# Optimization experiments

Hardware: AMD Instinct MI355X
Metric: run time of the kernel (lower is better)

Reference implementation:

```python
import jax, jax.numpy as jnp
import numpy as np

DOWNSAMPLE = 512  # points per cloud, from init_kwargs


def _pairwise_dist(x, y):
    """Batched Euclidean distance matrix. x: (B,n,D), y: (B,m,D) -> (B,n,m)."""
    x2 = jnp.sum(x * x, axis=-1)                     # (B,n)
    y2 = jnp.sum(y * y, axis=-1)                     # (B,m)
    d2 = x2[:, :, None] + y2[:, None, :] - 2.0 * jnp.einsum('bnd,bmd->bnm', x, y)
    pos = d2 > 0.0                                   # guard sqrt(0)/negatives from fp error
    return jnp.where(pos, jnp.sqrt(jnp.where(pos, d2, 1.0)), 0.0)


def setup_inputs() -> dict:
    key = jax.random.key(0)
    k1, k2 = jax.random.split(key)
    inp = jax.random.normal(k1, (65536, 128), dtype=jnp.float32)
    tgt = jax.random.normal(k2, (65536, 128), dtype=jnp.float32)
    return {"input": inp, "target": tgt}


def reference(input, target):
    D = input.shape[-1]
    x = input.reshape(-1, DOWNSAMPLE, D)   # (B, n, D)
    y = target.reshape(-1, DOWNSAMPLE, D)  # (B, n, D)
    # geomloss energy kernel loss with uniform weights:
    # L_b = mean||x-y|| - 0.5*mean||x-x'|| - 0.5*mean||y-y'||
    cross = jnp.mean(_pairwise_dist(x, y), axis=(1, 2))  # (B,)
    xx = jnp.mean(_pairwise_dist(x, x), axis=(1, 2))
    yy = jnp.mean(_pairwise_dist(y, y), axis=(1, 2))
    loss = cross - 0.5 * xx - 0.5 * yy
    return jnp.mean(loss)
```

## Files before the change

### kernel.cpp

```cpp
#include <hip/hip_runtime.h>

typedef __attribute__((ext_vector_type(8))) __bf16 bf16x8;
typedef __attribute__((ext_vector_type(4))) float f32x4;
typedef __attribute__((ext_vector_type(8))) unsigned short ushort8;
typedef __attribute__((ext_vector_type(4))) unsigned short u16x4;

#define DSAMP 512
#define DIM   128
#define S1    ((size_t)16777216)
#define REG5  16384
#define NBPB  36
#define WS_NEEDED ((size_t)(4 * S1 + 2 * 262144 + 128 * NBPB * 4))

__global__ __launch_bounds__(256)
void presplit3(const float* __restrict__ x, const float* __restrict__ y,
               char* __restrict__ ws) {
    __shared__ __align__(16) char img[4 * 8192];
    __shared__ float nrm[64];

    const int tid = threadIdx.x;
    const int nb  = gridDim.x >> 1;
    const int input = (blockIdx.x >= nb) ? 1 : 0;
    const int rb    = blockIdx.x - input * nb;

    const float* src = (input ? y : x) + (size_t)rb * 64 * DIM;

    #pragma unroll
    for (int i = 0; i < 8; ++i) {
        int f  = i * 256 + tid;
        int r  = f >> 5;
        int k4 = f & 31;
        float4 v = ((const float4*)src)[f];

        float s = v.x * v.x + v.y * v.y + v.z * v.z + v.w * v.w;
        #pragma unroll
        for (int o = 16; o > 0; o >>= 1) s += __shfl_down(s, o, 32);
        if ((tid & 31) == 0) nrm[r] = s;

        float xs[4] = {v.x, v.y, v.z, v.w};
        u16x4 hv, lv;
        #pragma unroll
        for (int e = 0; e < 4; ++e) {
            float xv = xs[e];
            unsigned ub = __float_as_uint(xv);
            unsigned hr = (ub + 0x7fffu + ((ub >> 16) & 1u)) >> 16;
            float hf = __uint_as_float(hr << 16);
            float rs = xv - hf;
            unsigned ul = __float_as_uint(rs);
            unsigned lr = (ul + 0x7fffu + ((ul >> 16) & 1u)) >> 16;
            hv[e] = (unsigned short)hr;
            lv[e] = (unsigned short)lr;
        }
        int c  = k4 >> 4;
        int q  = k4 & 15;
        int jb = q >> 1;
        int h  = q & 1;
        int addr = r * 128 + ((jb ^ (r & 7)) * 16) + h * 8;
        *(u16x4*)(img + (size_t)(0 + c) * 8192 + addr) = hv;
        *(u16x4*)(img + (size_t)(2 + c) * 8192 + addr) = lv;
    }
    __syncthreads();

    const int wv = tid >> 6, lane = tid & 63;
    const int hl = wv >> 1, ch = wv & 1;
    const int b     = rb >> 3;
    const int rowin = (rb & 7) * 64;
    char* gdst = ws + (size_t)input * 2 * S1 + (size_t)hl * S1
               + ((size_t)(b * 2 + ch) * 512 + rowin) * 128;
    const char* lsrc = img + (size_t)wv * 8192;
    #pragma unroll
    for (int j = 0; j < 8; ++j) {
        int o = (j * 64 + lane) * 16;
        *(float4*)(gdst + o) = *(const float4*)(lsrc + o);
    }
    if (tid < 64) {
        float* nG = (float*)(ws + 4 * S1) + (size_t)input * 65536 + rb * 64;
        nG[tid] = nrm[tid];
    }
}

__global__ __launch_bounds__(256, 3)
void mmd_tile5(const char* __restrict__ ws, float* __restrict__ partials) {
    __shared__ __align__(16) char smem[3 * REG5];
    __shared__ float Pn[128];
    __shared__ float Qn[128];
    __shared__ float wred[4];

    const int tid = threadIdx.x;
    const int xcd = blockIdx.x & 7;
    const int seq = blockIdx.x >> 3;
    const int b   = xcd + 8 * (seq / NBPB);
    const int s   = seq % NBPB;

    int type, ti, tj; float w; bool diag;
    if (s < 16) { type = 0; ti = s >> 2; tj = s & 3; w = 1.0f; diag = false; }
    else {
        int u = s - 16;
        type = 1 + (u >= 10);
        if (u >= 10) u -= 10;
        int i = (u >= 4) + (u >= 7) + (u >= 9);
        int off = (i == 1) ? 4 : (i == 2) ? 7 : (i == 3) ? 9 : 0;
        int j = u - off + i;
        ti = i; tj = j; diag = (i == j); w = diag ? -0.5f : -1.0f;
    }

    const char* Xhi = ws;
    const char* Yhi = ws + 2 * S1;
    const float* normX = (const float*)(ws + 4 * S1);
    const float* normY = normX + 65536;

    const char* Phi = (type == 2) ? Yhi : Xhi;
    const char* Qhi = (type == 1) ? Xhi : Yhi;
    const float* nP = (type == 2) ? normY : normX;
    const float* nQ = (type == 1) ? normX : normY;

    if (tid < 128) Pn[tid]       = nP[(size_t)b * 512 + ti * 128 + tid];
    else           Qn[tid - 128] = nQ[(size_t)b * 512 + tj * 128 + (tid - 128)];

    const int lane    = tid & 63;
    const int wv      = tid >> 6;
    const int rowHalf = (wv >> 1) * 64;
    const int colHalf = (wv & 1) * 64;
    const int fm      = lane & 15;
    const int kq      = lane >> 4;
    const int sw      = fm & 7;

    f32x4 acc[4][4];
    #pragma unroll
    for (int a2 = 0; a2 < 4; ++a2)
        #pragma unroll
        for (int b2 = 0; b2 < 4; ++b2)
            acc[a2][b2] = (f32x4){0.f, 0.f, 0.f, 0.f};

    for (int c = 0; c < 2; ++c) {
        if (c) __syncthreads();
        {
            size_t chrow = (size_t)(b * 2 + c) * 512;
            const char* srcs[3];
            srcs[0] = Phi + (chrow + (size_t)ti * 128) * 128;
            srcs[1] = Qhi + (chrow + (size_t)tj * 128) * 128;
            srcs[2] = srcs[1] + S1;
            #pragma unroll
            for (int f = 0; f < 12; ++f) {
                int g = wv * 12 + f;
                int region = g >> 4;
                int sub    = g & 15;
                const char* gs = srcs[region] + sub * 1024 + lane * 16;
                char* ls = smem + (size_t)region * REG5 + sub * 1024 + lane * 16;
                __builtin_amdgcn_global_load_lds(
                    (const __attribute__((address_space(1))) void*)gs,
                    (__attribute__((address_space(3))) void*)ls, 16, 0, 0);
            }
        }
        __syncthreads();
        #pragma unroll
        for (int ks = 0; ks < 2; ++ks) {
            const int jx = ((ks * 4 + kq) ^ sw) * 16;
            bf16x8 ah[4], bh[4], bl[4];
            #pragma unroll
            for (int a2 = 0; a2 < 4; ++a2) {
                int ar = rowHalf + a2 * 16 + fm;
                ah[a2] = *(const bf16x8*)(smem + ar * 128 + jx);
            }
            #pragma unroll
            for (int b2 = 0; b2 < 4; ++b2) {
                int br = colHalf + b2 * 16 + fm;
                bh[b2] = *(const bf16x8*)(smem + REG5     + br * 128 + jx);
                bl[b2] = *(const bf16x8*)(smem + 2 * REG5 + br * 128 + jx);
            }
            #pragma unroll
            for (int a2 = 0; a2 < 4; ++a2)
                #pragma unroll
                for (int b2 = 0; b2 < 4; ++b2) {
                    acc[a2][b2] = __builtin_amdgcn_mfma_f32_16x16x32_bf16(ah[a2], bh[b2], acc[a2][b2], 0, 0, 0);
                    acc[a2][b2] = __builtin_amdgcn_mfma_f32_16x16x32_bf16(ah[a2], bl[b2], acc[a2][b2], 0, 0, 0);
                }
        }
    }

    float Pr[16], Qc[4];
    #pragma unroll
    for (int a2 = 0; a2 < 4; ++a2)
        #pragma unroll
        for (int rg = 0; rg < 4; ++rg)
            Pr[a2 * 4 + rg] = Pn[rowHalf + a2 * 16 + kq * 4 + rg];
    #pragma unroll
    for (int b2 = 0; b2 < 4; ++b2) Qc[b2] = Qn[colHalf + b2 * 16 + fm];

    float lsum = 0.f;
    #pragma unroll
    for (int a2 = 0; a2 < 4; ++a2) {
        #pragma unroll
        for (int b2 = 0; b2 < 4; ++b2) {
            #pragma unroll
            for (int rg = 0; rg < 4; ++rg) {
                float d2 = fmaf(-2.0f, acc[a2][b2][rg], Pr[a2 * 4 + rg] + Qc[b2]);
                float v  = __builtin_amdgcn_sqrtf(fmaxf(d2, 0.0f));
                if (diag && (rowHalf + a2 * 16 + kq * 4 + rg) == (colHalf + b2 * 16 + fm))
                    v = 0.f;
                lsum += v;
            }
        }
    }
    #pragma unroll
    for (int off = 32; off > 0; off >>= 1) lsum += __shfl_down(lsum, off, 64);
    if (lane == 0) wred[wv] = lsum;
    __syncthreads();
    if (tid == 0)
        partials[blockIdx.x] = (wred[0] + wred[1] + wred[2] + wred[3]) * w;
}

__global__ __launch_bounds__(256, 2)
void mmd_tile_fallback(const float* __restrict__ x, const float* __restrict__ y,
                       float* __restrict__ partials) {
    __shared__ __align__(16) char smem[4 * 128 * 144];
    __shared__ float Pn[128];
    __shared__ float Qn[128];
    __shared__ float wred[4];

    char* Ah = smem;
    char* Al = smem + 1 * 128 * 144;
    char* Bh = smem + 2 * 128 * 144;
    char* Bl = smem + 3 * 128 * 144;

    const int tid  = threadIdx.x;
    const int bid  = blockIdx.x;
    const int tj   = bid & 3;
    const int ti   = (bid >> 2) & 3;
    const int type = (bid >> 4) % 3;
    const int b    = bid / 48;

    const float* Xb = x + (size_t)b * DSAMP * DIM;
    const float* Yb = y + (size_t)b * DSAMP * DIM;
    const float* Pp; const float* Qp; float w;
    if (type == 0)      { Pp = Xb; Qp = Yb; w = 1.0f;  }
    else if (type == 1) { Pp = Xb; Qp = Xb; w = -0.5f; }
    else                { Pp = Yb; Qp = Yb; w = -0.5f; }
    Pp += (size_t)ti * 128 * DIM;
    Qp += (size_t)tj * 128 * DIM;

    {
        const float* rp = (tid < 128) ? (Pp + (size_t)tid * DIM)
                                      : (Qp + (size_t)(tid - 128) * DIM);
        float s = 0.f;
        #pragma unroll
        for (int k4 = 0; k4 < 32; ++k4) {
            float4 v = ((const float4*)rp)[k4];
            s += v.x * v.x + v.y * v.y + v.z * v.z + v.w * v.w;
        }
        if (tid < 128) Pn[tid] = s; else Qn[tid - 128] = s;
    }

    const int lane    = tid & 63;
    const int wv      = tid >> 6;
    const int rowHalf = (wv >> 1) * 64;
    const int colHalf = (wv & 1) * 64;
    const int fm      = lane & 15;
    const int kq      = lane >> 4;

    f32x4 acc[4][4];
    #pragma unroll
    for (int a2 = 0; a2 < 4; ++a2)
        #pragma unroll
        for (int b2 = 0; b2 < 4; ++b2)
            acc[a2][b2] = (f32x4){0.f, 0.f, 0.f, 0.f};

    for (int c = 0; c < 2; ++c) {
        if (c) __syncthreads();
        #pragma unroll
        for (int side = 0; side < 2; ++side) {
            const float* sp = side ? Qp : Pp;
            char* dh = side ? Bh : Ah;
            char* dl = side ? Bl : Al;
            #pragma unroll
            for (int it = 0; it < 4; ++it) {
                int u  = it * 256 + tid;
                int r  = u >> 3;
                int c8 = u & 7;
                const float* g = sp + (size_t)r * DIM + c * 64 + c8 * 8;
                float4 v0 = ((const float4*)g)[0];
                float4 v1 = ((const float4*)g)[1];
                float xs[8] = {v0.x, v0.y, v0.z, v0.w, v1.x, v1.y, v1.z, v1.w};
                ushort8 hv, lv;
                #pragma unroll
                for (int e = 0; e < 8; ++e) {
                    float xv = xs[e];
                    unsigned ub = __float_as_uint(xv);
                    unsigned hr = (ub + 0x7fffu + ((ub >> 16) & 1u)) >> 16;
                    float hf = __uint_as_float(hr << 16);
                    float rs = xv - hf;
                    unsigned ul = __float_as_uint(rs);
                    unsigned lr = (ul + 0x7fffu + ((ul >> 16) & 1u)) >> 16;
                    hv[e] = (unsigned short)hr;
                    lv[e] = (unsigned short)lr;
                }
                *(ushort8*)(dh + r * 144 + c8 * 16) = hv;
                *(ushort8*)(dl + r * 144 + c8 * 16) = lv;
            }
        }
        __syncthreads();
        #pragma unroll
        for (int ks = 0; ks < 2; ++ks) {
            const int kb2 = (ks * 32 + kq * 8) * 2;
            bf16x8 ah[4], al[4], bh[4], bl[4];
            #pragma unroll
            for (int a2 = 0; a2 < 4; ++a2) {
                int ar = rowHalf + a2 * 16 + fm;
                ah[a2] = *(const bf16x8*)(Ah + ar * 144 + kb2);
                al[a2] = *(const bf16x8*)(Al + ar * 144 + kb2);
            }
            #pragma unroll
            for (int b2 = 0; b2 < 4; ++b2) {
                int br = colHalf + b2 * 16 + fm;
                bh[b2] = *(const bf16x8*)(Bh + br * 144 + kb2);
                bl[b2] = *(const bf16x8*)(Bl + br * 144 + kb2);
            }
            #pragma unroll
            for (int a2 = 0; a2 < 4; ++a2)
                #pragma unroll
                for (int b2 = 0; b2 < 4; ++b2) {
                    acc[a2][b2] = __builtin_amdgcn_mfma_f32_16x16x32_bf16(ah[a2], bh[b2], acc[a2][b2], 0, 0, 0);
                    acc[a2][b2] = __builtin_amdgcn_mfma_f32_16x16x32_bf16(ah[a2], bl[b2], acc[a2][b2], 0, 0, 0);
                    acc[a2][b2] = __builtin_amdgcn_mfma_f32_16x16x32_bf16(al[a2], bh[b2], acc[a2][b2], 0, 0, 0);
                }
        }
    }

    const bool selfm = (type != 0) && (ti == tj);
    float lsum = 0.f;
    #pragma unroll
    for (int a2 = 0; a2 < 4; ++a2) {
        int ib = rowHalf + a2 * 16 + kq * 4;
        #pragma unroll
        for (int b2 = 0; b2 < 4; ++b2) {
            int j = colHalf + b2 * 16 + fm;
            float qn = Qn[j];
            #pragma unroll
            for (int rg = 0; rg < 4; ++rg) {
                int i = ib + rg;
                float d2 = Pn[i] + qn - 2.0f * acc[a2][b2][rg];
                if (d2 > 0.f && !(selfm && i == j)) lsum += sqrtf(d2);
            }
        }
    }
    #pragma unroll
    for (int off = 32; off > 0; off >>= 1) lsum += __shfl_down(lsum, off, 64);
    if (lane == 0) wred[wv] = lsum;
    __syncthreads();
    if (tid == 0)
        partials[bid] = (wred[0] + wred[1] + wred[2] + wred[3]) * w;
}

__global__ __launch_bounds__(256)
void mmd_finalize_kernel(const float* __restrict__ partials, int n,
                         float* __restrict__ out, double scale) {
    __shared__ double sh[256];
    double s = 0.0;
    for (int i = threadIdx.x; i < n; i += 256) s += (double)partials[i];
    sh[threadIdx.x] = s;
    __syncthreads();
    for (int off = 128; off > 0; off >>= 1) {
        if ((int)threadIdx.x < off) sh[threadIdx.x] += sh[threadIdx.x + off];
        __syncthreads();
    }
    if (threadIdx.x == 0) out[0] = (float)(sh[0] * scale);
}

extern "C" void kernel_launch(void* const* d_in, const int* in_sizes, int n_in,
                              void* d_out, int out_size, void* d_ws, size_t ws_size,
                              hipStream_t stream) {
    const float* x = (const float*)d_in[0];
    const float* y = (const float*)d_in[1];
    float* out = (float*)d_out;

    const int n = in_sizes[0];
    const int B = n / (DSAMP * DIM);
    const double scale = 1.0 / ((double)B * (double)DSAMP * (double)DSAMP);

    if (ws_size >= WS_NEEDED) {
        char* ws = (char*)d_ws;
        float* partials = (float*)(ws + 4 * S1 + 2 * 262144);
        const int nb = (n / DIM) / 64;
        const int nblocks = B * NBPB;
        presplit3<<<dim3(2 * nb), dim3(256), 0, stream>>>(x, y, ws);
        mmd_tile5<<<dim3(nblocks), dim3(256), 0, stream>>>(ws, partials);
        mmd_finalize_kernel<<<dim3(1), dim3(256), 0, stream>>>(partials, nblocks, out, scale);
    } else {
        float* partials = (float*)d_ws;
        const int nblocks = B * 48;
        mmd_tile_fallback<<<dim3(nblocks), dim3(256), 0, stream>>>(x, y, partials);
        mmd_finalize_kernel<<<dim3(1), dim3(256), 0, stream>>>(partials, nblocks, out, scale);
    }
}
```

Measured before the change: 153.3 us.

## Load low-half B operand directly from global and simplify presplit kernel

The tile kernel no longer stages the low-order bf16 part of the Q operand in LDS. Each wave reads it straight from global memory into registers before the barrier, which cuts LDS to two regions and raises the occupancy hint from 3 to 4 blocks per CU. The presplit kernel drops its LDS staging and instead has each thread write swizzled hi/lo halves and norms directly to global memory. The trade-off is uncoalesced 8-byte global writes in presplit, and per-wave redundant, less-coalesced global reads of the lo tile in place of shared LDS reuse.

```diff
diff --git a/kernel.cpp b/kernel.cpp
--- a/kernel.cpp
+++ b/kernel.cpp
@@ -13,75 +13,59 @@
 #define WS_NEEDED ((size_t)(4 * S1 + 2 * 262144 + 128 * NBPB * 4))
 
 __global__ __launch_bounds__(256)
-void presplit3(const float* __restrict__ x, const float* __restrict__ y,
+void presplit4(const float* __restrict__ x, const float* __restrict__ y,
                char* __restrict__ ws) {
-    __shared__ __align__(16) char img[4 * 8192];
-    __shared__ float nrm[64];
-
     const int tid = threadIdx.x;
-    const int nb  = gridDim.x >> 1;
-    const int input = (blockIdx.x >= nb) ? 1 : 0;
-    const int rb    = blockIdx.x - input * nb;
-
-    const float* src = (input ? y : x) + (size_t)rb * 64 * DIM;
-
-    #pragma unroll
-    for (int i = 0; i < 8; ++i) {
-        int f  = i * 256 + tid;
-        int r  = f >> 5;
-        int k4 = f & 31;
-        float4 v = ((const float4*)src)[f];
-
-        float s = v.x * v.x + v.y * v.y + v.z * v.z + v.w * v.w;
-        #pragma unroll
-        for (int o = 16; o > 0; o >>= 1) s += __shfl_down(s, o, 32);
-        if ((tid & 31) == 0) nrm[r] = s;
-
-        float xs[4] = {v.x, v.y, v.z, v.w};
-        u16x4 hv, lv;
-        #pragma unroll
-        for (int e = 0; e < 4; ++e) {
-            float xv = xs[e];
-            unsigned ub = __float_as_uint(xv);
-            unsigned hr = (ub + 0x7fffu + ((ub >> 16) & 1u)) >> 16;
-            float hf = __uint_as_float(hr << 16);
-            float rs = xv - hf;
-            unsigned ul = __float_as_uint(rs);
-            unsigned lr = (ul + 0x7fffu + ((ul >> 16) & 1u)) >> 16;
-            hv[e] = (unsigned short)hr;
-            lv[e] = (unsigned short)lr;
-        }
-        int c  = k4 >> 4;
-        int q  = k4 & 15;
-        int jb = q >> 1;
-        int h  = q & 1;
-        int addr = r * 128 + ((jb ^ (r & 7)) * 16) + h * 8;
-        *(u16x4*)(img + (size_t)(0 + c) * 8192 + addr) = hv;
-        *(u16x4*)(img + (size_t)(2 + c) * 8192 + addr) = lv;
-    }
-    __syncthreads();
-
-    const int wv = tid >> 6, lane = tid & 63;
-    const int hl = wv >> 1, ch = wv & 1;
-    const int b     = rb >> 3;
-    const int rowin = (rb & 7) * 64;
-    char* gdst = ws + (size_t)input * 2 * S1 + (size_t)hl * S1
-               + ((size_t)(b * 2 + ch) * 512 + rowin) * 128;
-    const char* lsrc = img + (size_t)wv * 8192;
-    #pragma unroll
-    for (int j = 0; j < 8; ++j) {
-        int o = (j * 64 + lane) * 16;
-        *(float4*)(gdst + o) = *(const float4*)(lsrc + o);
-    }
-    if (tid < 64) {
-        float* nG = (float*)(ws + 4 * S1) + (size_t)input * 65536 + rb * 64;
-        nG[tid] = nrm[tid];
-    }
-}
-
-__global__ __launch_bounds__(256, 3)
-void mmd_tile5(const char* __restrict__ ws, float* __restrict__ partials) {
-    __shared__ __align__(16) char smem[3 * REG5];
+    const size_t fidx = (size_t)blockIdx.x * 256 + tid;
+    const int r   = (int)(fidx >> 5);
+    const int k4  = (int)(fidx & 31);
+    const int input = r >> 16;
+    const int ri    = r & 65535;
+
+    const float* src = input ? y : x;
+    float4 v = ((const float4*)src)[((size_t)ri << 5) + k4];
+
+    float s = v.x * v.x + v.y * v.y + v.z * v.z + v.w * v.w;
+    #pragma unroll
+    for (int o = 16; o > 0; o >>= 1) s += __shfl_down(s, o, 32);
+
+    float xs[4] = {v.x, v.y, v.z, v.w};
+    u16x4 hv, lv;
+    #pragma unroll
+    for (int e = 0; e < 4; ++e) {
+        float xv = xs[e];
+        unsigned ub = __float_as_uint(xv);
+        unsigned hr = (ub + 0x7fffu + ((ub >> 16) & 1u)) >> 16;
+        float hf = __uint_as_float(hr << 16);
+        float rs = xv - hf;
+        unsigned ul = __float_as_uint(rs);
+        unsigned lr = (ul + 0x7fffu + ((ul >> 16) & 1u)) >> 16;
+        hv[e] = (unsigned short)hr;
+        lv[e] = (unsigned short)lr;
+    }
+
+    const int b  = ri >> 9;
+    const int rb = ri & 511;
+    const int c  = k4 >> 4;
+    const int q  = k4 & 15;
+    const int jb = q >> 1;
+    const int h  = q & 1;
+    char* hi = ws + (size_t)input * 2 * S1;
+    char* lo = hi + S1;
+    size_t off = ((size_t)(b * 2 + c) * 512 + rb) * 128
+               + (size_t)((jb ^ (rb & 7)) * 16 + h * 8);
+    *(u16x4*)(hi + off) = hv;
+    *(u16x4*)(lo + off) = lv;
+
+    if (k4 == 0) {
+        float* nG = (float*)(ws + 4 * S1) + (size_t)input * 65536;
+        nG[ri] = s;
+    }
+}
+
+__global__ __launch_bounds__(256, 4)
+void mmd_tile6(const char* __restrict__ ws, float* __restrict__ partials) {
+    __shared__ __align__(16) char smem[2 * REG5];
     __shared__ float Pn[128];
     __shared__ float Qn[128];
     __shared__ float wred[4];
@@ -111,6 +95,7 @@
 
     const char* Phi = (type == 2) ? Yhi : Xhi;
     const char* Qhi = (type == 1) ? Xhi : Yhi;
+    const char* Qlo = Qhi + S1;
     const float* nP = (type == 2) ? normY : normX;
     const float* nQ = (type == 1) ? normX : normY;
 
@@ -134,15 +119,14 @@
 
     for (int c = 0; c < 2; ++c) {
         if (c) __syncthreads();
+        size_t chrow = (size_t)(b * 2 + c) * 512;
         {
-            size_t chrow = (size_t)(b * 2 + c) * 512;
-            const char* srcs[3];
+            const char* srcs[2];
             srcs[0] = Phi + (chrow + (size_t)ti * 128) * 128;
             srcs[1] = Qhi + (chrow + (size_t)tj * 128) * 128;
-            srcs[2] = srcs[1] + S1;
-            #pragma unroll
-            for (int f = 0; f < 12; ++f) {
-                int g = wv * 12 + f;
+            #pragma unroll
+            for (int f = 0; f < 8; ++f) {
+                int g = wv * 8 + f;
                 int region = g >> 4;
                 int sub    = g & 15;
                 const char* gs = srcs[region] + sub * 1024 + lane * 16;
@@ -152,11 +136,21 @@
                     (__attribute__((address_space(3))) void*)ls, 16, 0, 0);
             }
         }
-        __syncthreads();
+        bf16x8 bl[2][4];
         #pragma unroll
         for (int ks = 0; ks < 2; ++ks) {
             const int jx = ((ks * 4 + kq) ^ sw) * 16;
-            bf16x8 ah[4], bh[4], bl[4];
+            #pragma unroll
+            for (int b2 = 0; b2 < 4; ++b2) {
+                size_t br = (size_t)(colHalf + b2 * 16 + fm);
+                bl[ks][b2] = *(const bf16x8*)(Qlo + ((chrow + tj * 128 + br) << 7) + jx);
+            }
+        }
+        __syncthreads();
+        #pragma unroll
+        for (int ks = 0; ks < 2; ++ks) {
+            const int jx = ((ks * 4 + kq) ^ sw) * 16;
+            bf16x8 ah[4], bh[4];
             #pragma unroll
             for (int a2 = 0; a2 < 4; ++a2) {
                 int ar = rowHalf + a2 * 16 + fm;
@@ -165,15 +159,14 @@
             #pragma unroll
             for (int b2 = 0; b2 < 4; ++b2) {
                 int br = colHalf + b2 * 16 + fm;
-                bh[b2] = *(const bf16x8*)(smem + REG5     + br * 128 + jx);
-                bl[b2] = *(const bf16x8*)(smem + 2 * REG5 + br * 128 + jx);
+                bh[b2] = *(const bf16x8*)(smem + REG5 + br * 128 + jx);
             }
             #pragma unroll
             for (int a2 = 0; a2 < 4; ++a2)
                 #pragma unroll
                 for (int b2 = 0; b2 < 4; ++b2) {
                     acc[a2][b2] = __builtin_amdgcn_mfma_f32_16x16x32_bf16(ah[a2], bh[b2], acc[a2][b2], 0, 0, 0);
-                    acc[a2][b2] = __builtin_amdgcn_mfma_f32_16x16x32_bf16(ah[a2], bl[b2], acc[a2][b2], 0, 0, 0);
+                    acc[a2][b2] = __builtin_amdgcn_mfma_f32_16x16x32_bf16(ah[a2], bl[ks][b2], acc[a2][b2], 0, 0, 0);
                 }
         }
     }
@@ -380,10 +373,10 @@
     if (ws_size >= WS_NEEDED) {
         char* ws = (char*)d_ws;
         float* partials = (float*)(ws + 4 * S1 + 2 * 262144);
-        const int nb = (n / DIM) / 64;
+        const int nf4 = (2 * n) / 4;
         const int nblocks = B * NBPB;
-        presplit3<<<dim3(2 * nb), dim3(256), 0, stream>>>(x, y, ws);
-        mmd_tile5<<<dim3(nblocks), dim3(256), 0, stream>>>(ws, partials);
+        presplit4<<<dim3(nf4 / 256), dim3(256), 0, stream>>>(x, y, ws);
+        mmd_tile6<<<dim3(nblocks), dim3(256), 0, stream>>>(ws, partials);
         mmd_finalize_kernel<<<dim3(1), dim3(256), 0, stream>>>(partials, nblocks, out, scale);
     } else {
         float* partials = (float*)d_ws;
```

After: 228.4 us. +49.0%, slower.
